# Kernel tuning notes

Hardware: AMD Instinct MI355X
Metric: run time of the kernel (lower is better)

Reference implementation:

```python
import jax, jax.numpy as jnp
import numpy as np

BINS = 10          # par.BINS
ALPHA = 0.5        # par.RATIO_KLD
EPS = 1e-10
NUM_ENC = 10       # encoded feature columns used for histograms
BLOCKS = ((7, 19), (19, 21), (21, 25), (25, 27), (27, 29), (29, 31), (31, 34), (34, 38), (38, 50))
B = 1048576


def setup_inputs() -> dict:
    key = jax.random.key(0)
    ks = jax.random.split(key, 16)
    data_encoded = jax.random.normal(ks[0], (B, NUM_ENC), dtype=jnp.float32)
    data_decoded = jax.random.normal(ks[1], (B, 50), dtype=jnp.float32)
    parts = [jax.random.normal(ks[2], (B, 7), dtype=jnp.float32)]  # numerical part
    for i, (s, e) in enumerate(BLOCKS):  # one-hot categorical ground truth
        lab = jax.random.randint(ks[3 + i], (B,), 0, e - s)
        parts.append(jax.nn.one_hot(lab, e - s, dtype=jnp.float32))
    data_true = jnp.concatenate(parts, axis=1)  # (B, 50)
    grp = jax.random.randint(ks[12], (B,), 0, 2).astype(jnp.float32)  # marital flag -> column 11 of combined
    label_true = jnp.stack([
        jax.random.randint(ks[13], (B,), 0, 2).astype(jnp.float32),
        grp,
        jax.random.normal(ks[14], (B,), dtype=jnp.float32),
    ], axis=1)  # (B, 3)
    return {"data_encoded": data_encoded, "data_decoded": data_decoded,
            "data_true": data_true, "label_true": label_true, "batch_size": B}


def _ce(logits, onehot):
    # F.cross_entropy with labels recovered from one-hot rows (nonzero -> argmax)
    labels = jnp.argmax(onehot, axis=1)
    lp = jax.nn.log_softmax(logits, axis=1)
    return -jnp.mean(jnp.take_along_axis(lp, labels[:, None], axis=1))


def _group_hist(enc, mask, mins, maxs):
    # torch.histc per column, restricted to rows where mask==1, normalized by group size
    width = jnp.maximum(maxs - mins, EPS)
    bins = jnp.clip(jnp.floor((enc - mins) / width * BINS), 0, BINS - 1).astype(jnp.int32)  # (B, 10)
    flat = bins + jnp.arange(NUM_ENC, dtype=jnp.int32)[None, :] * BINS                     # (B, 10)
    w = jnp.broadcast_to(mask[:, None], flat.shape).reshape(-1)
    hist = jnp.zeros(NUM_ENC * BINS, dtype=jnp.float32).at[flat.reshape(-1)].add(w)
    return hist.reshape(NUM_ENC, BINS) / jnp.maximum(jnp.sum(mask), 1.0)


def _kl(p, q):
    # KL(p || q) summed over all (feature, bin) cells, zero-safe
    return jnp.sum(jnp.where(p > 0, p * jnp.log(p / jnp.maximum(q, EPS)), 0.0))


def reference(data_encoded, data_decoded, data_true, label_true, batch_size):
    # numerical MSE over first 7 cols, then *7 (mse_Loss)
    mse_loss = jnp.mean((data_decoded[:, 0:7] - data_true[:, 0:7]) ** 2) * 7.0
    # 9 cross-entropy terms over categorical blocks
    ce_loss = jnp.float32(0.0)
    for s, e in BLOCKS:
        ce_loss = ce_loss + _ce(data_decoded[:, s:e], data_true[:, s:e])
    # per-group histogram KLD over the 10 encoded columns (detached in the original)
    enc = data_encoded  # first 10 cols of encoded_combined
    mins = jnp.min(enc, axis=0)
    maxs = jnp.max(enc, axis=0)
    grp = label_true[:, 1]  # column 11 of cat(data_encoded, label_true)
    single_mask = (grp == 0).astype(jnp.float32)
    married_mask = (grp == 1).astype(jnp.float32)
    p = _group_hist(enc, single_mask, mins, maxs)   # (10, BINS)
    q = _group_hist(enc, married_mask, mins, maxs)  # (10, BINS)
    kld = jax.lax.stop_gradient(_kl(p, q))  # original goes through .numpy() -> no grads
    multi_loss = (1.0 - ALPHA) * (mse_loss + ce_loss) + ALPHA * kld
    return (multi_loss, mse_loss, ce_loss, ALPHA * kld)
```

## Files before the change

### kernel.cpp

```cpp
#include <hip/hip_runtime.h>
#include <math.h>

#define EPSF 1e-10f
#define TILE 32
#define TILEH 64

struct WS {
  double sum_mse, sum_ce;
  float mn[10], mx[10];
};

typedef __attribute__((address_space(3))) unsigned int lds_u32_t;
typedef __attribute__((address_space(1))) const unsigned int glb_u32_t;
__device__ __forceinline__ void load_lds16(const void* g, void* l){
  __builtin_amdgcn_global_load_lds((glb_u32_t*)g, (lds_u32_t*)l, 16, 0, 0);
}

template<int S, int E>
__device__ __forceinline__ float ce_block_lds(const float* __restrict__ d,
                                              const float* __restrict__ t){
  constexpr int N = E - S;
  float dv[N];
  #pragma unroll
  for (int j = 0; j < N; j++) dv[j] = d[S + j];
  float mx = dv[0];
  #pragma unroll
  for (int j = 1; j < N; j++) mx = fmaxf(mx, dv[j]);
  float se = 0.f, dot = 0.f;
  #pragma unroll
  for (int j = 0; j < N; j++){ se += __expf(dv[j] - mx); dot += t[S + j] * dv[j]; }
  return mx + __logf(se) - dot;
}

__global__ void k_main(const float* __restrict__ enc, const float* __restrict__ dec,
                       const float* __restrict__ tru,
                       double* __restrict__ pmMse, double* __restrict__ pmCe,
                       float* __restrict__ pmMn, float* __restrict__ pmMx,
                       int B, int nbm){
  __shared__ alignas(16) float bufD[TILE * 50];
  __shared__ alignas(16) float bufT[TILE * 50];
  __shared__ alignas(16) float bufE[TILE * 10];
  __shared__ double sMse[4], sCe[4];
  __shared__ float  sMn[4][10], sMx[4][10];

  const int tid  = threadIdx.x;
  const int wave = tid >> 6;
  const int lane = tid & 63;
  const int h    = tid >> 5;
  const int row  = tid & 31;

  float mn[10], mx[10];
  #pragma unroll
  for (int c = 0; c < 10; c++){ mn[c] = 3.4e38f; mx[c] = -3.4e38f; }
  float mse_acc = 0.f, ce_acc = 0.f;

  const int nTiles = (B + TILE - 1) / TILE;

  auto stage = [&](int tl){
    const int rowsHere = min(TILE, B - tl * TILE);
    const size_t base50 = (size_t)tl * TILE * 50;
    const size_t base10 = (size_t)tl * TILE * 10;
    if (rowsHere == TILE){
      const float4* dp4 = reinterpret_cast<const float4*>(dec + base50);
      const float4* tp4 = reinterpret_cast<const float4*>(tru + base50);
      const float4* ep4 = reinterpret_cast<const float4*>(enc + base10);
      float4* bD = reinterpret_cast<float4*>(bufD);
      float4* bT = reinterpret_cast<float4*>(bufT);
      float4* bE = reinterpret_cast<float4*>(bufE);
      #pragma unroll
      for (int k = 0; k < 2; k++){
        int i = tid + k * 256;
        if (i < 400){ load_lds16(dp4 + i, bD + i); }
      }
      #pragma unroll
      for (int k = 0; k < 2; k++){
        int i = tid + k * 256;
        if (i < 400){ load_lds16(tp4 + i, bT + i); }
      }
      { int i = tid; if (i < 80){ load_lds16(ep4 + i, bE + i); } }
    } else {
      const int nf = rowsHere * 50, ne = rowsHere * 10;
      for (int i = tid; i < nf; i += 256){ bufD[i] = dec[base50 + i]; bufT[i] = tru[base50 + i]; }
      for (int i = tid; i < ne; i += 256){ bufE[i] = enc[base10 + i]; }
    }
  };

  for (int tl = blockIdx.x; tl < nTiles; tl += nbm){
    stage(tl);
    __syncthreads();

    const int rowsHere = min(TILE, B - tl * TILE);
    if (row < rowsHere){
      const float* d = bufD + row * 50;
      const float* t = bufT + row * 50;
      const float* e = bufE + row * 10;
      switch (h){
        case 0: {
          float m = 0.f;
          #pragma unroll
          for (int j = 0; j < 7; j++){ float df = d[j] - t[j]; m += df * df; }
          mse_acc += m;
          { float v = e[0]; mn[0] = fminf(mn[0], v); mx[0] = fmaxf(mx[0], v); }
          { float v = e[1]; mn[1] = fminf(mn[1], v); mx[1] = fmaxf(mx[1], v); }
        } break;
        case 1: {
          ce_acc += ce_block_lds< 7,19>(d, t);
          { float v = e[2]; mn[2] = fminf(mn[2], v); mx[2] = fmaxf(mx[2], v); }
        } break;
        case 2: {
          ce_acc += ce_block_lds<19,21>(d, t);
          ce_acc += ce_block_lds<21,25>(d, t);
          { float v = e[3]; mn[3] = fminf(mn[3], v); mx[3] = fmaxf(mx[3], v); }
        } break;
        case 3: {
          ce_acc += ce_block_lds<25,27>(d, t);
          ce_acc += ce_block_lds<27,29>(d, t);
          { float v = e[4]; mn[4] = fminf(mn[4], v); mx[4] = fmaxf(mx[4], v); }
        } break;
        case 4: {
          ce_acc += ce_block_lds<29,31>(d, t);
          ce_acc += ce_block_lds<31,34>(d, t);
          { float v = e[5]; mn[5] = fminf(mn[5], v); mx[5] = fmaxf(mx[5], v); }
          { float v = e[6]; mn[6] = fminf(mn[6], v); mx[6] = fmaxf(mx[6], v); }
        } break;
        case 5: {
          ce_acc += ce_block_lds<34,38>(d, t);
          { float v = e[7]; mn[7] = fminf(mn[7], v); mx[7] = fmaxf(mx[7], v); }
        } break;
        case 6: {
          ce_acc += ce_block_lds<38,50>(d, t);
          { float v = e[8]; mn[8] = fminf(mn[8], v); mx[8] = fmaxf(mx[8], v); }
        } break;
        default: {
          { float v = e[9]; mn[9] = fminf(mn[9], v); mx[9] = fmaxf(mx[9], v); }
        } break;
      }
    }
    __syncthreads();
  }

  #pragma unroll
  for (int c = 0; c < 10; c++){
    #pragma unroll
    for (int o = 32; o >= 1; o >>= 1){
      mn[c] = fminf(mn[c], __shfl_xor(mn[c], o));
      mx[c] = fmaxf(mx[c], __shfl_xor(mx[c], o));
    }
  }
  double mseD = (double)mse_acc, ceD = (double)ce_acc;
  #pragma unroll
  for (int o = 32; o >= 1; o >>= 1){
    mseD += __shfl_xor(mseD, o);
    ceD  += __shfl_xor(ceD,  o);
  }
  if (lane == 0){
    sMse[wave] = mseD; sCe[wave] = ceD;
    #pragma unroll
    for (int c = 0; c < 10; c++){ sMn[wave][c] = mn[c]; sMx[wave][c] = mx[c]; }
  }
  __syncthreads();
  if (tid == 0){
    pmMse[blockIdx.x] = sMse[0] + sMse[1] + sMse[2] + sMse[3];
    pmCe[blockIdx.x]  = sCe[0]  + sCe[1]  + sCe[2]  + sCe[3];
    #pragma unroll
    for (int c = 0; c < 10; c++){
      pmMn[c * nbm + blockIdx.x] = fminf(fminf(sMn[0][c], sMn[1][c]), fminf(sMn[2][c], sMn[3][c]));
      pmMx[c * nbm + blockIdx.x] = fmaxf(fmaxf(sMx[0][c], sMx[1][c]), fmaxf(sMx[2][c], sMx[3][c]));
    }
  }
}

__global__ void k_reduce(const double* __restrict__ pmMse, const double* __restrict__ pmCe,
                         const float* __restrict__ pmMn, const float* __restrict__ pmMx,
                         WS* __restrict__ ws, int nbm){
  __shared__ double sM[16], sC[16];
  __shared__ float  sMn[16][10], sMx[16][10];
  const int tid  = threadIdx.x;
  const int wave = tid >> 6;
  const int lane = tid & 63;

  double ms = 0.0, ce = 0.0;
  float mn[10], mx[10];
  #pragma unroll
  for (int c = 0; c < 10; c++){ mn[c] = 3.4e38f; mx[c] = -3.4e38f; }
  for (int i = tid; i < nbm; i += 1024){
    ms += pmMse[i]; ce += pmCe[i];
    #pragma unroll
    for (int c = 0; c < 10; c++){
      mn[c] = fminf(mn[c], pmMn[c * nbm + i]);
      mx[c] = fmaxf(mx[c], pmMx[c * nbm + i]);
    }
  }
  #pragma unroll
  for (int o = 32; o >= 1; o >>= 1){
    ms += __shfl_xor(ms, o);
    ce += __shfl_xor(ce, o);
    #pragma unroll
    for (int c = 0; c < 10; c++){
      mn[c] = fminf(mn[c], __shfl_xor(mn[c], o));
      mx[c] = fmaxf(mx[c], __shfl_xor(mx[c], o));
    }
  }
  if (lane == 0){
    sM[wave] = ms; sC[wave] = ce;
    #pragma unroll
    for (int c = 0; c < 10; c++){ sMn[wave][c] = mn[c]; sMx[wave][c] = mx[c]; }
  }
  __syncthreads();
  if (tid == 0){
    double tm = 0.0, tc = 0.0;
    float rmn[10], rmx[10];
    #pragma unroll
    for (int c = 0; c < 10; c++){ rmn[c] = 3.4e38f; rmx[c] = -3.4e38f; }
    #pragma unroll
    for (int w = 0; w < 16; w++){
      tm += sM[w]; tc += sC[w];
      #pragma unroll
      for (int c = 0; c < 10; c++){
        rmn[c] = fminf(rmn[c], sMn[w][c]);
        rmx[c] = fmaxf(rmx[c], sMx[w][c]);
      }
    }
    ws->sum_mse = tm; ws->sum_ce = tc;
    #pragma unroll
    for (int c = 0; c < 10; c++){ ws->mn[c] = rmn[c]; ws->mx[c] = rmx[c]; }
  }
}

__global__ void k_hist(const float* __restrict__ enc, const float* __restrict__ lab,
                       const WS* __restrict__ ws, unsigned* __restrict__ ph,
                       int B, int nbh){
  __shared__ unsigned int sh[202];
  __shared__ alignas(16) float bufE[2][TILEH * 10];
  __shared__ alignas(16) float bufL[2][TILEH * 3];

  const int tid  = threadIdx.x;
  const int wave = tid >> 6;
  const int lane = tid & 63;

  for (int i = tid; i < 202; i += 256) sh[i] = 0u;

  float mnv[10], wv[10];
  #pragma unroll
  for (int c = 0; c < 10; c++){
    float lo = ws->mn[c];
    float hi = ws->mx[c];
    mnv[c] = lo;
    wv[c]  = fmaxf(hi - lo, EPSF);
  }

  const int nTiles = (B + TILEH - 1) / TILEH;

  auto stage = [&](int b, int tl){
    const int rowsHere = min(TILEH, B - tl * TILEH);
    const size_t base10 = (size_t)tl * TILEH * 10;
    const size_t base3  = (size_t)tl * TILEH * 3;
    if (rowsHere == TILEH){
      const float4* ep4 = reinterpret_cast<const float4*>(enc + base10);
      const float4* lp4 = reinterpret_cast<const float4*>(lab + base3);
      float4* bE = reinterpret_cast<float4*>(bufE[b]);
      float4* bL = reinterpret_cast<float4*>(bufL[b]);
      { int i = tid; if (i < 160) load_lds16(ep4 + i, bE + i); }
      { int i = tid; if (i < 48)  load_lds16(lp4 + i, bL + i); }
    } else {
      const int ne = rowsHere * 10, nl = rowsHere * 3;
      for (int i = tid; i < ne; i += 256) bufE[b][i] = enc[base10 + i];
      for (int i = tid; i < nl; i += 256) bufL[b][i] = lab[base3 + i];
    }
  };

  const int t0 = blockIdx.x;
  if (t0 < nTiles) stage(0, t0);
  __syncthreads();

  int cur = 0;
  for (int tl = t0; tl < nTiles; tl += nbh){
    int nxt = tl + nbh;
    if (nxt < nTiles) stage(cur ^ 1, nxt);

    const int rowsHere = min(TILEH, B - tl * TILEH);
    const int rrow = lane;
    if (rrow < rowsHere){
      float g = bufL[cur][rrow * 3 + 1];
      int gi = (g == 0.0f) ? 0 : ((g == 1.0f) ? 1 : -1);
      if (gi >= 0){
        const float* e = bufE[cur] + rrow * 10;
        if (wave == 1) atomicAdd(&sh[200 + gi], 1u);
        #define DO_BIN(c) { \
          float bf = floorf((e[(c)] - mnv[(c)]) / wv[(c)] * 10.0f); \
          int b2 = (int)bf; b2 = b2 < 0 ? 0 : (b2 > 9 ? 9 : b2); \
          atomicAdd(&sh[gi * 100 + (c) * 10 + b2], 1u); }
        if (wave == 0){ DO_BIN(0) DO_BIN(1) DO_BIN(2) }
        else if (wave == 1){ DO_BIN(3) DO_BIN(4) }
        else if (wave == 2){ DO_BIN(5) DO_BIN(6) }
        else { DO_BIN(7) DO_BIN(8) DO_BIN(9) }
        #undef DO_BIN
      }
    }
    __syncthreads();
    cur ^= 1;
  }

  for (int i = tid; i < 202; i += 256) ph[(size_t)i * nbh + blockIdx.x] = sh[i];
}

__global__ void k_hreduce(const unsigned* __restrict__ ph, float* __restrict__ histF, int nbh){
  __shared__ unsigned swv[4];
  const int e    = blockIdx.x;
  const int tid  = threadIdx.x;
  const int wave = tid >> 6;
  const int lane = tid & 63;
  const unsigned* p = ph + (size_t)e * nbh;
  unsigned s0 = 0, s1 = 0, s2 = 0, s3 = 0;
  int k = tid;
  for (; k + 768 < nbh; k += 1024){
    s0 += p[k]; s1 += p[k + 256]; s2 += p[k + 512]; s3 += p[k + 768];
  }
  for (; k < nbh; k += 256) s0 += p[k];
  unsigned s = s0 + s1 + s2 + s3;
  #pragma unroll
  for (int o = 32; o >= 1; o >>= 1) s += __shfl_xor(s, o);
  if (lane == 0) swv[wave] = s;
  __syncthreads();
  if (tid == 0) histF[e] = (float)(swv[0] + swv[1] + swv[2] + swv[3]);
}

__global__ void k_final(const float* __restrict__ histF, const WS* __restrict__ ws,
                        float* __restrict__ out, int B){
  const int tid = threadIdx.x;
  float dens = fmaxf(histF[200], 1.0f);
  float denm = fmaxf(histF[201], 1.0f);
  float kl = 0.f;
  for (int i = tid; i < 100; i += 64){
    float p = histF[i]       / dens;
    float q = histF[100 + i] / denm;
    if (p > 0.f) kl += p * logf(p / fmaxf(q, EPSF));
  }
  #pragma unroll
  for (int o = 32; o >= 1; o >>= 1) kl += __shfl_xor(kl, o);
  if (tid == 0){
    float mse = (float)(ws->sum_mse / (double)B);
    float ce  = (float)(ws->sum_ce  / (double)B);
    float akld = 0.5f * kl;
    out[0] = 0.5f * (mse + ce) + akld;
    out[1] = mse;
    out[2] = ce;
    out[3] = akld;
  }
}

extern "C" void kernel_launch(void* const* d_in, const int* in_sizes, int n_in,
                              void* d_out, int out_size, void* d_ws, size_t ws_size,
                              hipStream_t stream){
  const float* enc = (const float*)d_in[0];
  const float* dec = (const float*)d_in[1];
  const float* tru = (const float*)d_in[2];
  const float* lab = (const float*)d_in[3];
  int B = in_sizes[1] / 50;

  int nbm = 2048, nbh = 2048;
  while ((size_t)(128 + (size_t)nbm * 96 + (size_t)202 * nbh * 4 + 1024) > ws_size && nbm > 64){
    nbm >>= 1; nbh >>= 1;
  }
  char* w = (char*)d_ws;
  WS* ws = (WS*)w;
  double* pmMse = (double*)(w + 128);
  double* pmCe  = (double*)(w + 128 + (size_t)nbm * 8);
  float*  pmMn  = (float*)(w + 128 + (size_t)nbm * 16);
  float*  pmMx  = (float*)(w + 128 + (size_t)nbm * 16 + (size_t)nbm * 40);
  unsigned* ph  = (unsigned*)(w + 128 + (size_t)nbm * 96);
  float* histF  = (float*)(w + 128 + (size_t)nbm * 96 + (size_t)202 * nbh * 4);
  float* out = (float*)d_out;

  hipLaunchKernelGGL(k_main,    dim3(nbm), dim3(256),  0, stream, enc, dec, tru,
                     pmMse, pmCe, pmMn, pmMx, B, nbm);
  hipLaunchKernelGGL(k_reduce,  dim3(1),   dim3(1024), 0, stream, pmMse, pmCe, pmMn, pmMx, ws, nbm);
  hipLaunchKernelGGL(k_hist,    dim3(nbh), dim3(256),  0, stream, enc, lab, ws, ph, B, nbh);
  hipLaunchKernelGGL(k_hreduce, dim3(202), dim3(256),  0, stream, ph, histF, nbh);
  hipLaunchKernelGGL(k_final,   dim3(1),   dim3(64),   0, stream, histF, ws, out, B);
}
```

Baseline: 127.1 us.

## Double-buffer main kernel tiles via register prefetch and cut grid size

The main loss kernel now prefetches the next tile's decoded, true and encoded rows into registers while the current tile is computed from a second LDS buffer. This replaces the direct global-to-LDS loads and removes one barrier per tile. The grid shrinks from 2048 to 1280 blocks, and a generic fallback kernel handles batch sizes that are not a multiple of the tile. The trade-off is more LDS and register pressure, and the global loads now pass through VGPRs instead of going straight to LDS.

Result: faster. 121.6 us, median of 2 (-4.3%).

```diff
diff --git a/kernel.cpp b/kernel.cpp
--- a/kernel.cpp
+++ b/kernel.cpp
@@ -5,10 +5,7 @@
 #define TILE 32
 #define TILEH 64
 
-struct WS {
-  double sum_mse, sum_ce;
-  float mn[10], mx[10];
-};
+struct WS { double sum_mse, sum_ce; float mn[10], mx[10]; };
 
 typedef __attribute__((address_space(3))) unsigned int lds_u32_t;
 typedef __attribute__((address_space(1))) const unsigned int glb_u32_t;
@@ -37,9 +34,9 @@
                        double* __restrict__ pmMse, double* __restrict__ pmCe,
                        float* __restrict__ pmMn, float* __restrict__ pmMx,
                        int B, int nbm){
-  __shared__ alignas(16) float bufD[TILE * 50];
-  __shared__ alignas(16) float bufT[TILE * 50];
-  __shared__ alignas(16) float bufE[TILE * 10];
+  __shared__ alignas(16) float bufD[2][TILE * 50];
+  __shared__ alignas(16) float bufT[2][TILE * 50];
+  __shared__ alignas(16) float bufE[2][TILE * 10];
   __shared__ double sMse[4], sCe[4];
   __shared__ float  sMn[4][10], sMx[4][10];
 
@@ -54,46 +51,43 @@
   for (int c = 0; c < 10; c++){ mn[c] = 3.4e38f; mx[c] = -3.4e38f; }
   float mse_acc = 0.f, ce_acc = 0.f;
 
-  const int nTiles = (B + TILE - 1) / TILE;
-
-  auto stage = [&](int tl){
-    const int rowsHere = min(TILE, B - tl * TILE);
-    const size_t base50 = (size_t)tl * TILE * 50;
-    const size_t base10 = (size_t)tl * TILE * 10;
-    if (rowsHere == TILE){
-      const float4* dp4 = reinterpret_cast<const float4*>(dec + base50);
-      const float4* tp4 = reinterpret_cast<const float4*>(tru + base50);
-      const float4* ep4 = reinterpret_cast<const float4*>(enc + base10);
-      float4* bD = reinterpret_cast<float4*>(bufD);
-      float4* bT = reinterpret_cast<float4*>(bufT);
-      float4* bE = reinterpret_cast<float4*>(bufE);
-      #pragma unroll
-      for (int k = 0; k < 2; k++){
-        int i = tid + k * 256;
-        if (i < 400){ load_lds16(dp4 + i, bD + i); }
-      }
-      #pragma unroll
-      for (int k = 0; k < 2; k++){
-        int i = tid + k * 256;
-        if (i < 400){ load_lds16(tp4 + i, bT + i); }
-      }
-      { int i = tid; if (i < 80){ load_lds16(ep4 + i, bE + i); } }
-    } else {
-      const int nf = rowsHere * 50, ne = rowsHere * 10;
-      for (int i = tid; i < nf; i += 256){ bufD[i] = dec[base50 + i]; bufT[i] = tru[base50 + i]; }
-      for (int i = tid; i < ne; i += 256){ bufE[i] = enc[base10 + i]; }
-    }
+  const int nTiles = B / TILE;
+  int nT_loc = (blockIdx.x < nTiles) ? (nTiles - blockIdx.x + nbm - 1) / nbm : 0;
+
+  float4 rd0, rd1, rt0, rt1, re;
+
+  auto load_stage = [&](int k){
+    const int tl = blockIdx.x + k * nbm;
+    const float4* dp4 = reinterpret_cast<const float4*>(dec + (size_t)tl * (TILE * 50));
+    const float4* tp4 = reinterpret_cast<const float4*>(tru + (size_t)tl * (TILE * 50));
+    const float4* ep4 = reinterpret_cast<const float4*>(enc + (size_t)tl * (TILE * 10));
+    rd0 = dp4[tid];
+    rt0 = tp4[tid];
+    if (tid < 144){ rd1 = dp4[256 + tid]; rt1 = tp4[256 + tid]; }
+    if (tid < 80){ re = ep4[tid]; }
   };
-
-  for (int tl = blockIdx.x; tl < nTiles; tl += nbm){
-    stage(tl);
+  auto write_stage = [&](int b){
+    float4* bD = reinterpret_cast<float4*>(bufD[b]);
+    float4* bT = reinterpret_cast<float4*>(bufT[b]);
+    float4* bE = reinterpret_cast<float4*>(bufE[b]);
+    bD[tid] = rd0;
+    bT[tid] = rt0;
+    if (tid < 144){ bD[256 + tid] = rd1; bT[256 + tid] = rt1; }
+    if (tid < 80){ bE[tid] = re; }
+  };
+
+  if (nT_loc > 0) load_stage(0);
+
+  for (int k = 0; k < nT_loc; ++k){
+    const int b = k & 1;
+    write_stage(b);
+    if (k + 1 < nT_loc) load_stage(k + 1);
     __syncthreads();
 
-    const int rowsHere = min(TILE, B - tl * TILE);
-    if (row < rowsHere){
-      const float* d = bufD + row * 50;
-      const float* t = bufT + row * 50;
-      const float* e = bufE + row * 10;
+    {
+      const float* d = bufD[b] + row * 50;
+      const float* t = bufT[b] + row * 50;
+      const float* e = bufE[b] + row * 10;
       switch (h){
         case 0: {
           float m = 0.f;
@@ -136,7 +130,6 @@
         } break;
       }
     }
-    __syncthreads();
   }
 
   #pragma unroll
@@ -153,6 +146,68 @@
     mseD += __shfl_xor(mseD, o);
     ceD  += __shfl_xor(ceD,  o);
   }
+  __syncthreads();
+  if (lane == 0){
+    sMse[wave] = mseD; sCe[wave] = ceD;
+    #pragma unroll
+    for (int c = 0; c < 10; c++){ sMn[wave][c] = mn[c]; sMx[wave][c] = mx[c]; }
+  }
+  __syncthreads();
+  if (tid == 0){
+    pmMse[blockIdx.x] = sMse[0] + sMse[1] + sMse[2] + sMse[3];
+    pmCe[blockIdx.x]  = sCe[0]  + sCe[1]  + sCe[2]  + sCe[3];
+    #pragma unroll
+    for (int c = 0; c < 10; c++){
+      pmMn[c * nbm + blockIdx.x] = fminf(fminf(sMn[0][c], sMn[1][c]), fminf(sMn[2][c], sMn[3][c]));
+      pmMx[c * nbm + blockIdx.x] = fmaxf(fmaxf(sMx[0][c], sMx[1][c]), fmaxf(sMx[2][c], sMx[3][c]));
+    }
+  }
+}
+
+__global__ void k_main_fb(const float* __restrict__ enc, const float* __restrict__ dec,
+                          const float* __restrict__ tru,
+                          double* __restrict__ pmMse, double* __restrict__ pmCe,
+                          float* __restrict__ pmMn, float* __restrict__ pmMx,
+                          int B, int nbm){
+  __shared__ double sMse[4], sCe[4];
+  __shared__ float  sMn[4][10], sMx[4][10];
+  const int tid = threadIdx.x, wave = tid >> 6, lane = tid & 63;
+  float mn[10], mx[10];
+  #pragma unroll
+  for (int c = 0; c < 10; c++){ mn[c] = 3.4e38f; mx[c] = -3.4e38f; }
+  float mse_acc = 0.f, ce_acc = 0.f;
+  int stride = nbm * 256;
+  for (int r = blockIdx.x * 256 + tid; r < B; r += stride){
+    const float* e = enc + (size_t)r * 10;
+    #pragma unroll
+    for (int c = 0; c < 10; c++){ float v = e[c]; mn[c] = fminf(mn[c], v); mx[c] = fmaxf(mx[c], v); }
+    const float* d = dec + (size_t)r * 50;
+    const float* t = tru + (size_t)r * 50;
+    float m = 0.f;
+    #pragma unroll
+    for (int j = 0; j < 7; j++){ float df = d[j] - t[j]; m += df * df; }
+    mse_acc += m;
+    ce_acc += ce_block_lds< 7,19>(d, t);
+    ce_acc += ce_block_lds<19,21>(d, t);
+    ce_acc += ce_block_lds<21,25>(d, t);
+    ce_acc += ce_block_lds<25,27>(d, t);
+    ce_acc += ce_block_lds<27,29>(d, t);
+    ce_acc += ce_block_lds<29,31>(d, t);
+    ce_acc += ce_block_lds<31,34>(d, t);
+    ce_acc += ce_block_lds<34,38>(d, t);
+    ce_acc += ce_block_lds<38,50>(d, t);
+  }
+  #pragma unroll
+  for (int c = 0; c < 10; c++){
+    #pragma unroll
+    for (int o = 32; o >= 1; o >>= 1){
+      mn[c] = fminf(mn[c], __shfl_xor(mn[c], o));
+      mx[c] = fmaxf(mx[c], __shfl_xor(mx[c], o));
+    }
+  }
+  double mseD = (double)mse_acc, ceD = (double)ce_acc;
+  #pragma unroll
+  for (int o = 32; o >= 1; o >>= 1){ mseD += __shfl_xor(mseD, o); ceD += __shfl_xor(ceD, o); }
   if (lane == 0){
     sMse[wave] = mseD; sCe[wave] = ceD;
     #pragma unroll
@@ -175,10 +230,7 @@
                          WS* __restrict__ ws, int nbm){
   __shared__ double sM[16], sC[16];
   __shared__ float  sMn[16][10], sMx[16][10];
-  const int tid  = threadIdx.x;
-  const int wave = tid >> 6;
-  const int lane = tid & 63;
-
+  const int tid = threadIdx.x, wave = tid >> 6, lane = tid & 63;
   double ms = 0.0, ce = 0.0;
   float mn[10], mx[10];
   #pragma unroll
@@ -193,8 +245,7 @@
   }
   #pragma unroll
   for (int o = 32; o >= 1; o >>= 1){
-    ms += __shfl_xor(ms, o);
-    ce += __shfl_xor(ce, o);
+    ms += __shfl_xor(ms, o); ce += __shfl_xor(ce, o);
     #pragma unroll
     for (int c = 0; c < 10; c++){
       mn[c] = fminf(mn[c], __shfl_xor(mn[c], o));
@@ -212,8 +263,8 @@
     float rmn[10], rmx[10];
     #pragma unroll
     for (int c = 0; c < 10; c++){ rmn[c] = 3.4e38f; rmx[c] = -3.4e38f; }
-    #pragma unroll
-    for (int w = 0; w < 16; w++){
+    const int nw = (int)(blockDim.x >> 6);
+    for (int w = 0; w < nw; w++){
       tm += sM[w]; tc += sC[w];
       #pragma unroll
       for (int c = 0; c < 10; c++){
@@ -306,10 +357,7 @@
 
 __global__ void k_hreduce(const unsigned* __restrict__ ph, float* __restrict__ histF, int nbh){
   __shared__ unsigned swv[4];
-  const int e    = blockIdx.x;
-  const int tid  = threadIdx.x;
-  const int wave = tid >> 6;
-  const int lane = tid & 63;
+  const int e = blockIdx.x, tid = threadIdx.x, wave = tid >> 6, lane = tid & 63;
   const unsigned* p = ph + (size_t)e * nbh;
   unsigned s0 = 0, s1 = 0, s2 = 0, s3 = 0;
   int k = tid;
@@ -358,7 +406,18 @@
   const float* lab = (const float*)d_in[3];
   int B = in_sizes[1] / 50;
 
-  int nbm = 2048, nbh = 2048;
+  const bool fast = (B > 0) && (B % TILE == 0);
+
+  int nbm = 1280;
+  int nTm = fast ? (B / TILE) : ((B + 255) / 256);
+  if (nbm > nTm && nTm > 0) nbm = nTm;
+  if (nbm < 1) nbm = 1;
+
+  int nbh = 2048;
+  int nTh = (B + TILEH - 1) / TILEH;
+  if (nbh > nTh && nTh > 0) nbh = nTh;
+  if (nbh < 1) nbh = 1;
+
   while ((size_t)(128 + (size_t)nbm * 96 + (size_t)202 * nbh * 4 + 1024) > ws_size && nbm > 64){
     nbm >>= 1; nbh >>= 1;
   }
@@ -372,8 +431,12 @@
   float* histF  = (float*)(w + 128 + (size_t)nbm * 96 + (size_t)202 * nbh * 4);
   float* out = (float*)d_out;
 
-  hipLaunchKernelGGL(k_main,    dim3(nbm), dim3(256),  0, stream, enc, dec, tru,
-                     pmMse, pmCe, pmMn, pmMx, B, nbm);
+  if (fast)
+    hipLaunchKernelGGL(k_main,    dim3(nbm), dim3(256), 0, stream, enc, dec, tru,
+                       pmMse, pmCe, pmMn, pmMx, B, nbm);
+  else
+    hipLaunchKernelGGL(k_main_fb, dim3(nbm), dim3(256), 0, stream, enc, dec, tru,
+                       pmMse, pmCe, pmMn, pmMx, B, nbm);
   hipLaunchKernelGGL(k_reduce,  dim3(1),   dim3(1024), 0, stream, pmMse, pmCe, pmMn, pmMx, ws, nbm);
   hipLaunchKernelGGL(k_hist,    dim3(nbh), dim3(256),  0, stream, enc, lab, ws, ph, B, nbh);
   hipLaunchKernelGGL(k_hreduce, dim3(202), dim3(256),  0, stream, ph, histF, nbh);
```
